# Kernel tuning notes

Hardware: AMD Instinct MI355X
Metric: run time of the kernel (lower is better)

The kernel has to match this reference:

```python
import jax, jax.numpy as jnp
import numpy as np

N = 10000          # nodes
E = 320000         # edges
C = 128            # num_features (channels per irrep)
RB = 8             # radial basis size
NS = 10            # num_species
HID = 64           # radial MLP hidden
NPATH = 5          # TP paths: 0x0->0, 0x1->1, 1x0->1, 1x1->0(dot), 1x1->1(cross)
EPS = 0.17677669529663687  # 1/sqrt(avg_degree=32)


def setup_inputs() -> dict:
    key = jax.random.key(0)
    ks = jax.random.split(key, 20)
    inp = {
        "vectors": jax.random.normal(ks[0], (E, 3), jnp.float32),
        "node_feats": jax.random.normal(ks[1], (N, C * 4), jnp.float32),
        "node_specie": jax.random.randint(ks[2], (N,), 0, NS),
        "radial_embedding": jax.random.normal(ks[3], (E, RB), jnp.float32),
        "senders": jax.random.randint(ks[4], (E,), 0, N),
        "receivers": jax.random.randint(ks[5], (E,), 0, N),
    }
    s = 1.0 / np.sqrt(C)
    inp["W_up_s"] = jax.random.normal(ks[6], (C, C), jnp.float32) * s
    inp["W_up_v"] = jax.random.normal(ks[7], (C, C), jnp.float32) * s
    inp["W_rad1"] = jax.random.normal(ks[8], (RB, HID), jnp.float32) / np.sqrt(RB)
    inp["W_rad2"] = jax.random.normal(ks[9], (HID, NPATH * C), jnp.float32) / np.sqrt(HID)
    inp["W_down_s"] = jax.random.normal(ks[10], (C, C), jnp.float32) * s
    inp["W_down_v"] = jax.random.normal(ks[11], (C, C), jnp.float32) * s
    inp["W_skip_s"] = jax.random.normal(ks[12], (NS, C, C), jnp.float32) * s
    inp["W_skip_v"] = jax.random.normal(ks[13], (NS, C, C), jnp.float32) * s
    inp["W_prod_s"] = jax.random.normal(ks[14], (NS, 3, C), jnp.float32)
    inp["W_prod_v"] = jax.random.normal(ks[15], (NS, 2, C), jnp.float32)
    inp["W_lin_s"] = jax.random.normal(ks[16], (C, C), jnp.float32) * s
    inp["W_lin_v"] = jax.random.normal(ks[17], (C, C), jnp.float32) * s
    inp["W_ro"] = jax.random.normal(ks[18], (C, 1), jnp.float32) * s
    return inp


def _mace_forward(vectors, node_feats, node_specie, radial_embedding, senders,
                  receivers, W_up_s, W_up_v, W_rad1, W_rad2, W_down_s, W_down_v,
                  W_skip_s, W_skip_v, W_prod_s, W_prod_v, W_lin_s, W_lin_v, W_ro):
    n = node_feats.shape[0]
    # split flat mul_ir layout: [C x 0e | C x 1o]
    s = node_feats[:, :C]                      # [N, C]
    v = node_feats[:, C:].reshape(n, C, 3)     # [N, C, 3]

    # --- skip connection (species-indexed linear, first=False) ---
    Ws = W_skip_s[node_specie]                 # [N, C, C]
    Wv = W_skip_v[node_specie]
    sc_s = jnp.einsum('nc,ncd->nd', s, Ws)
    sc_v = jnp.einsum('nci,ncd->ndi', v, Wv)

    # --- interaction: linear_up ---
    h_s = s @ W_up_s
    h_v = jnp.einsum('nci,cd->ndi', v, W_up_v)

    # spherical harmonics (component normalization): Y1 = sqrt(3)*r_hat
    norm = jnp.linalg.norm(vectors, axis=-1, keepdims=True)
    Y1 = jnp.sqrt(3.0) * vectors / (norm + 1e-9)           # [E, 3]

    # radial MLP -> per-edge, per-path, per-channel TP weights
    w = jax.nn.silu(radial_embedding @ W_rad1) @ W_rad2
    w = w.reshape(-1, NPATH, C)                            # [E, 5, C]

    # gather sender features, depthwise ('uvu') CG tensor product with Y
    s_j = h_s[senders]                                     # [E, C]
    v_j = h_v[senders]                                     # [E, C, 3]
    dot = jnp.einsum('eci,ei->ec', v_j, Y1)                # 1o x 1o -> 0e
    crs = jnp.cross(v_j, Y1[:, None, :])                   # 1o x 1o -> 1o
    m_s = w[:, 0] * s_j + w[:, 3] * dot                    # [E, C]
    m_v = (w[:, 1][:, :, None] * s_j[:, :, None] * Y1[:, None, :]
           + w[:, 2][:, :, None] * v_j
           + w[:, 4][:, :, None] * crs)                    # [E, C, 3]

    # scatter to receivers
    agg_s = jax.ops.segment_sum(m_s, receivers, num_segments=n)
    agg_v = jax.ops.segment_sum(m_v, receivers, num_segments=n)

    # linear_down + epsilon scaling
    f_s = (agg_s @ W_down_s) * EPS
    f_v = jnp.einsum('nci,cd->ndi', agg_v, W_down_v) * EPS

    # --- equivariant product basis (correlation=2, symmetric) ---
    # order-1 and order-2 symmetric contractions for (0e, 1o) inputs:
    # scalars: A_s, A_s^2, |A_v|^2 ; vectors: A_v, A_s * A_v
    B_s = jnp.stack([f_s, f_s * f_s, jnp.sum(f_v * f_v, axis=-1)], axis=1)  # [N,3,C]
    B_v = jnp.stack([f_v, f_s[:, :, None] * f_v], axis=1)                    # [N,2,C,3]
    p_s = jnp.einsum('nkc,nkc->nc', B_s, W_prod_s[node_specie])
    p_v = jnp.einsum('nkci,nkc->nci', B_v, W_prod_v[node_specie])
    out_s = p_s @ W_lin_s + sc_s
    out_v = jnp.einsum('nci,cd->ndi', p_v, W_lin_v) + sc_v

    # --- linear readout (not last layer): invariant 0e output ---
    node_outputs = out_s @ W_ro                            # [N, 1]
    new_feats = jnp.concatenate([out_s, out_v.reshape(n, C * 3)], axis=-1)
    return node_outputs, new_feats


def reference(vectors, node_feats, node_specie, radial_embedding, senders,
              receivers, W_up_s, W_up_v, W_rad1, W_rad2, W_down_s, W_down_v,
              W_skip_s, W_skip_v, W_prod_s, W_prod_v, W_lin_s, W_lin_v, W_ro):
    return _mace_forward(vectors, node_feats, node_specie, radial_embedding,
                         senders, receivers, W_up_s, W_up_v, W_rad1, W_rad2,
                         W_down_s, W_down_v, W_skip_s, W_skip_v, W_prod_s,
                         W_prod_v, W_lin_s, W_lin_v, W_ro)
```

## Files before the change

kernel.cpp:

```cpp
#include <hip/hip_runtime.h>
#include <hip/hip_bf16.h>


#define NN 10000
#define EE 320000
#define FEPS 0.17677669529663687f

typedef __attribute__((ext_vector_type(4))) float f32x4;
typedef __attribute__((ext_vector_type(8))) short s16x8;

__device__ __forceinline__ float bflo(unsigned u) { return __uint_as_float(u << 16); }
__device__ __forceinline__ float bfhi(unsigned u) { return __uint_as_float(u & 0xffff0000u); }
__device__ __forceinline__ unsigned short f2bu(float f) {
    unsigned u = __float_as_uint(f);
    return (unsigned short)((u + 0x7FFFu + ((u >> 16) & 1u)) >> 16);
}
__device__ __forceinline__ unsigned pack2(float a, float b) {
    return (unsigned)f2bu(a) | ((unsigned)f2bu(b) << 16);
}
__device__ __forceinline__ s16x8 pack8(float4 a, float4 b) {
    union { s16x8 v; unsigned short u[8]; } r;
    r.u[0] = f2bu(a.x); r.u[1] = f2bu(a.y); r.u[2] = f2bu(a.z); r.u[3] = f2bu(a.w);
    r.u[4] = f2bu(b.x); r.u[5] = f2bu(b.y); r.u[6] = f2bu(b.z); r.u[7] = f2bu(b.w);
    return r.v;
}

#define TWN (26 * 16384)
#define W2N (640 * 64)
#define PREPX 20
#define HISTB 1250
__global__ __launch_bounds__(256) void k_prep_hist(
    const float* __restrict__ Wus, const float* __restrict__ Wuv,
    const float* __restrict__ Wds, const float* __restrict__ Wdv,
    const float* __restrict__ Wls, const float* __restrict__ Wlv,
    const float* __restrict__ Wss, const float* __restrict__ Wsv,
    const float* __restrict__ W_rad2,
    unsigned short* __restrict__ T,
    unsigned short* __restrict__ w2t,
    const int* __restrict__ recv, int* __restrict__ cnt) {
    const int b = blockIdx.x, tid = threadIdx.x;
    if (b < 26) {
        __shared__ unsigned short tr[128][130];
        const int m = b;
        const float* src;
        if (m == 0) src = Wus; else if (m == 1) src = Wuv;
        else if (m == 2) src = Wds; else if (m == 3) src = Wdv;
        else if (m == 4) src = Wls; else if (m == 5) src = Wlv;
        else if (m < 16) src = Wss + (size_t)(m - 6) * 16384;
        else src = Wsv + (size_t)(m - 16) * 16384;
        for (int i = tid; i < 16384; i += 256) {
            const int c = i >> 7, d = i & 127;
            tr[d][c] = f2bu(src[i]);
        }
        __syncthreads();
        unsigned* o32 = (unsigned*)(T + (size_t)m * 16384);
        for (int i = tid; i < 8192; i += 256) {
            const int d = i >> 6, c2 = (i & 63) * 2;
            o32[i] = (unsigned)tr[d][c2] | ((unsigned)tr[d][c2 + 1] << 16);
        }
    } else if (b < 26 + PREPX) {
        for (int i = (b - 26) * 256 + tid; i < W2N; i += PREPX * 256) {
            const int n = i >> 6, k = i & 63;
            w2t[i] = f2bu(W_rad2[k * 640 + n]);
        }
    } else {
        const int e = (b - (26 + PREPX)) * 256 + tid;
        if (e < EE) {
            int r = recv[e];
            r = ((unsigned)r < NN) ? r : 0;
            atomicAdd(&cnt[r], 1);
        }
    }
}

__global__ __launch_bounds__(1024) void k_scan_spec(
    const int* __restrict__ cnt, int* __restrict__ offs, int* __restrict__ cur,
    const int* __restrict__ specie, int* __restrict__ perm,
    int2* __restrict__ tiles, int* __restrict__ ntiles) {
    __shared__ int sums[1024];
    __shared__ int hcnt[10], hbase[10], hcur[10], tbase[11];
    const int t = threadIdx.x;
    const int chunk = (NN + 1023) / 1024;
    const int start = t * chunk;
    int local = 0;
    for (int i = 0; i < chunk; i++) {
        int idx = start + i;
        if (idx < NN) local += cnt[idx];
    }
    sums[t] = local;
    __syncthreads();
    for (int ofs = 1; ofs < 1024; ofs <<= 1) {
        int u = (t >= ofs) ? sums[t - ofs] : 0;
        __syncthreads();
        sums[t] += u;
        __syncthreads();
    }
    int base = (t == 0) ? 0 : sums[t - 1];
    for (int i = 0; i < chunk; i++) {
        int idx = start + i;
        if (idx < NN) {
            offs[idx] = base;
            cur[idx] = base;
            base += cnt[idx];
        }
    }
    if (t == 0) offs[NN] = sums[1023];
    if (t < 10) hcnt[t] = 0;
    __syncthreads();
    for (int n = t; n < NN; n += 1024) {
        int s = specie[n];
        s = ((unsigned)s < 10) ? s : 0;
        atomicAdd(&hcnt[s], 1);
    }
    __syncthreads();
    if (t == 0) {
        int run = 0, tc = 0;
        for (int sp = 0; sp < 10; sp++) {
            hbase[sp] = run; hcur[sp] = run; run += hcnt[sp];
            tbase[sp] = tc;  tc += (hcnt[sp] + 15) >> 4;
        }
        tbase[10] = tc;
        *ntiles = tc;
    }
    __syncthreads();
    const int tc = tbase[10];
    for (int ti = t; ti < tc; ti += 1024) {
        int sp = 0;
        while (sp < 9 && ti >= tbase[sp + 1]) sp++;
        const int b = (ti - tbase[sp]) * 16;
        tiles[ti] = make_int2(hbase[sp] + b, (sp << 8) | min(16, hcnt[sp] - b));
    }
    for (int n = t; n < NN; n += 1024) {
        int s = specie[n];
        s = ((unsigned)s < 10) ? s : 0;
        int slot = atomicAdd(&hcur[s], 1);
        if ((unsigned)slot < NN) perm[slot] = n;
    }
}

__global__ __launch_bounds__(256) void k_fill_pre(
    const int* __restrict__ recv, int* __restrict__ cur, int* __restrict__ csr,
    const float* __restrict__ nf,
    const unsigned short* __restrict__ Tw,
    uint2* __restrict__ h4o) {
    if (blockIdx.x >= 625) {
        const int e = (blockIdx.x - 625) * 256 + threadIdx.x;
        if (e < EE) {
            int r = recv[e];
            r = ((unsigned)r < NN) ? r : 0;
            int slot = atomicAdd(&cur[r], 1);
            if ((unsigned)slot < EE) csr[slot] = e;
        }
        return;
    }
    const int tile = blockIdx.x;
    const int tid = threadIdx.x;
    const int lane = tid & 63, wv = tid >> 6;
    const int col = lane & 15, quad = lane >> 4;
    __shared__ float nfl[16][512];
    {
        const float4* src = (const float4*)(nf + (size_t)tile * 16 * 512);
        float4* dst = (float4*)nfl;
        for (int i = tid; i < 2048; i += 256) dst[i] = src[i];
    }
    __syncthreads();
    const float* rp = nfl[col];
    s16x8 Af[4][4];
#pragma unroll
    for (int kt = 0; kt < 4; kt++) {
        const int ko = kt * 32 + quad * 8;
        const float4 fa = *(const float4*)(rp + ko);
        const float4 fb = *(const float4*)(rp + ko + 4);
        Af[0][kt] = pack8(fa, fb);
#pragma unroll
        for (int i = 0; i < 3; i++) {
            union { s16x8 v; unsigned short u[8]; } A;
#pragma unroll
            for (int j = 0; j < 8; j++) A.u[j] = f2bu(rp[128 + 3 * (ko + j) + i]);
            Af[1 + i][kt] = A.v;
        }
    }
    const unsigned short* Ts = Tw;
    const unsigned short* Tv = Tw + 16384;
#pragma unroll
    for (int nt = 0; nt < 2; nt++) {
        const int d = 32 * wv + 16 * nt + col;
        f32x4 C[4];
#pragma unroll
        for (int m = 0; m < 4; m++) C[m] = (f32x4){0.f, 0.f, 0.f, 0.f};
#pragma unroll
        for (int kt = 0; kt < 4; kt++) {
            const int ko = kt * 32 + quad * 8;
            const s16x8 Bs = *(const s16x8*)&Ts[(size_t)d * 128 + ko];
            const s16x8 Bv = *(const s16x8*)&Tv[(size_t)d * 128 + ko];
            C[0] = __builtin_amdgcn_mfma_f32_16x16x32_bf16(Af[0][kt], Bs, C[0], 0, 0, 0);
#pragma unroll
            for (int i = 0; i < 3; i++)
                C[1 + i] = __builtin_amdgcn_mfma_f32_16x16x32_bf16(Af[1 + i][kt], Bv, C[1 + i], 0, 0, 0);
        }
        const int P = ((d >> 5) << 4) + (d & 15);
        const int half = (d >> 4) & 1;
#pragma unroll
        for (int reg = 0; reg < 4; reg++) {
            const int node = tile * 16 + quad * 4 + reg;
            h4o[((size_t)node * 64 + P) * 2 + half] =
                make_uint2(pack2(C[0][reg], C[1][reg]), pack2(C[2][reg], C[3][reg]));
        }
    }
}

#define EGRID 2560
__global__ __launch_bounds__(256, 2) void k_edge_mfma(
    const float* __restrict__ vectors,
    const float* __restrict__ radial,
    const int* __restrict__ senders,
    const float* __restrict__ W_rad1,
    const unsigned short* __restrict__ w2t,
    const uint4* __restrict__ h4q,
    const int* __restrict__ offs, const int* __restrict__ csr,
    unsigned short* __restrict__ aggb) {
    __shared__ unsigned short w1s[512];
    __shared__ float4 em[3][64];
    __shared__ float radl[3][64][8];
    __shared__ unsigned short hidb[2 * 64 * 72];
    const int tid = threadIdx.x;
    const int lane = tid & 63, wv = tid >> 6;
    const int row = lane & 15, quad = lane >> 4;
    const int sE = tid >> 2, st = tid & 3;
    for (int i = tid; i < 512; i += 256) w1s[i] = f2bu(W_rad1[i]);

    s16x8 Bf[2][5][2];
#pragma unroll
    for (int ti = 0; ti < 2; ti++) {
        const int t = 2 * wv + ti;
#pragma unroll
        for (int p = 0; p < 5; p++) {
            const unsigned short* bp =
                w2t + (size_t)(128 * p + 16 * t + row) * 64 + quad * 8;
            Bf[ti][p][0] = *(const s16x8*)(bp);
            Bf[ti][p][1] = *(const s16x8*)(bp + 32);
        }
    }

    int curN = blockIdx.x, curS = offs[curN], curD = offs[curN + 1] - curS, curC0 = 0;
    int nxtN = curN, nxtS = curS, nxtD = curD, nxtC0 = 0;
    {
        nxtC0 += 64;
        if (nxtC0 >= nxtD) {
            nxtN += EGRID;
            if (nxtN < NN) { nxtS = offs[nxtN]; nxtD = offs[nxtN + 1] - nxtS; }
            nxtC0 = 0;
        }
    }
    int nx2N = nxtN, nx2S = nxtS, nx2D = nxtD, nx2C0 = nxtC0;
    if (nx2N < NN) {
        nx2C0 += 64;
        if (nx2C0 >= nx2D) {
            nx2N += EGRID;
            if (nx2N < NN) { nx2S = offs[nx2N]; nx2D = offs[nx2N + 1] - nx2S; }
            nx2C0 = 0;
        }
    }

    if (st < 2) {
        const int gi = curC0 + sE;
        if (gi < curD) {
            int e = csr[curS + gi];
            e = ((unsigned)e < EE) ? e : 0;
            if (st == 0) {
                int j = senders[e];
                j = ((unsigned)j < NN) ? j : 0;
                const float vx = vectors[e * 3 + 0];
                const float vy = vectors[e * 3 + 1];
                const float vz = vectors[e * 3 + 2];
                const float inr = 1.7320508075688772f /
                    (sqrtf(vx * vx + vy * vy + vz * vz) + 1e-9f);
                em[0][sE] = make_float4(__int_as_float(j), vx * inr, vy * inr, vz * inr);
            } else {
                *(float4*)&radl[0][sE][0] = *(const float4*)(radial + (size_t)e * 8);
                *(float4*)&radl[0][sE][4] = *(const float4*)(radial + (size_t)e * 8 + 4);
            }
        } else {
            if (st == 0) em[0][sE] = make_float4(0.f, 0.f, 0.f, 0.f);
            else {
                *(float4*)&radl[0][sE][0] = make_float4(0.f, 0.f, 0.f, 0.f);
                *(float4*)&radl[0][sE][4] = make_float4(0.f, 0.f, 0.f, 0.f);
            }
        }
    }
    int eReg = -1;
    if (nxtN < NN && st < 2) {
        const int gi = nxtC0 + sE;
        if (gi < nxtD) {
            int e = csr[nxtS + gi];
            eReg = ((unsigned)e < EE) ? e : 0;
        }
    }
    __syncthreads();

    float acc_s[2] = {0.f, 0.f}, av0[2] = {0.f, 0.f},
          av1[2] = {0.f, 0.f}, av2[2] = {0.f, 0.f};
    int cs = 0, hbI = 0;
    while (true) {
        const int ws = (cs == 2) ? 0 : cs + 1;
        const bool hasNxt = (nxtN < NN);
        const float4* emc = em[cs];
        const float* emf = (const float*)emc;
        uint4 hqA[4];
#pragma unroll
        for (int rg = 0; rg < 4; rg++) {
            const int j = __float_as_int(emf[(quad * 4 + rg) * 4]);
            hqA[rg] = h4q[(size_t)j * 64 + (wv << 4) + row];
        }
        bool sv = false;
        float4 ra0 = make_float4(0.f, 0.f, 0.f, 0.f);
        float4 ra1 = make_float4(0.f, 0.f, 0.f, 0.f);
        if (hasNxt && st < 2 && eReg >= 0) {
            sv = true;
            const int e = eReg;
            if (st == 0) {
                int j = senders[e];
                j = ((unsigned)j < NN) ? j : 0;
                ra0 = make_float4(vectors[e * 3 + 0], vectors[e * 3 + 1],
                                  vectors[e * 3 + 2], __int_as_float(j));
            } else {
                ra0 = *(const float4*)(radial + (size_t)e * 8);
                ra1 = *(const float4*)(radial + (size_t)e * 8 + 4);
            }
        }
        int eRegN = -1;
        if (nx2N < NN && st < 2) {
            const int gi = nx2C0 + sE;
            if (gi < nx2D) {
                int e = csr[nx2S + gi];
                eRegN = ((unsigned)e < EE) ? e : 0;
            }
        }
        const int glimC = min(64, curD - curC0);
        {
            const int g16C = (glimC + 15) & ~15;
            unsigned short* hb = hidb + hbI * 4608;
            const int u0 = st * 16;
            if (sE < glimC) {
                float rr[8];
                *(float4*)&rr[0] = *(const float4*)&radl[cs][sE][0];
                *(float4*)&rr[4] = *(const float4*)&radl[cs][sE][4];
#pragma unroll
                for (int h = 0; h < 2; h++) {
                    float a[8];
#pragma unroll
                    for (int u = 0; u < 8; u++) a[u] = 0.f;
#pragma unroll
                    for (int r = 0; r < 8; r++) {
                        const uint4 wa = *(const uint4*)&w1s[r * 64 + u0 + h * 8];
                        const float f = rr[r];
                        a[0] += f * bflo(wa.x); a[1] += f * bfhi(wa.x);
                        a[2] += f * bflo(wa.y); a[3] += f * bfhi(wa.y);
                        a[4] += f * bflo(wa.z); a[5] += f * bfhi(wa.z);
                        a[6] += f * bflo(wa.w); a[7] += f * bfhi(wa.w);
                    }
                    unsigned o[4];
#pragma unroll
                    for (int k = 0; k < 4; k++) {
                        const float s0 = a[2 * k] / (1.f + __expf(-a[2 * k]));
                        const float s1 = a[2 * k + 1] / (1.f + __expf(-a[2 * k + 1]));
                        o[k] = pack2(s0, s1);
                    }
                    *(uint4*)&hb[sE * 72 + u0 + h * 8] = make_uint4(o[0], o[1], o[2], o[3]);
                }
            } else if (sE < g16C) {
                *(uint4*)&hb[sE * 72 + u0] = make_uint4(0, 0, 0, 0);
                *(uint4*)&hb[sE * 72 + u0 + 8] = make_uint4(0, 0, 0, 0);
            }
        }
        if (hasNxt && st < 2) {
            if (st == 0) {
                if (sv) {
                    const float vx = ra0.x, vy = ra0.y, vz = ra0.z;
                    const float inr = 1.7320508075688772f /
                        (sqrtf(vx * vx + vy * vy + vz * vz) + 1e-9f);
                    em[ws][sE] = make_float4(ra0.w, vx * inr, vy * inr, vz * inr);
                } else {
                    em[ws][sE] = make_float4(0.f, 0.f, 0.f, 0.f);
                }
            } else {
                *(float4*)&radl[ws][sE][0] = ra0;
                *(float4*)&radl[ws][sE][4] = ra1;
            }
        }
        __syncthreads();
        {
            __builtin_amdgcn_s_setprio(1);
            const unsigned short* hb = hidb + hbI * 4608;
            for (int g0 = 0; g0 < glimC; g0 += 16) {
                const s16x8 A0 = *(const s16x8*)&hb[(g0 + row) * 72 + quad * 8];
                const s16x8 A1 = *(const s16x8*)&hb[(g0 + row) * 72 + 32 + quad * 8];
                float4 mm[4];
#pragma unroll
                for (int rg = 0; rg < 4; rg++) mm[rg] = emc[g0 + quad * 4 + rg];
                const bool more = (g0 + 16) < glimC;
                uint4 hqB[4];
                if (more) {
#pragma unroll
                    for (int rg = 0; rg < 4; rg++) {
                        const int j = __float_as_int(emf[(g0 + 16 + quad * 4 + rg) * 4]);
                        hqB[rg] = h4q[(size_t)j * 64 + (wv << 4) + row];
                    }
                }
#pragma unroll
                for (int ti = 0; ti < 2; ti++) {
                    float sj[4], a0r[4], a1r[4], a2r[4];
#pragma unroll
                    for (int rg = 0; rg < 4; rg++) {
                        const unsigned wx = ti ? hqA[rg].z : hqA[rg].x;
                        const unsigned wy = ti ? hqA[rg].w : hqA[rg].y;
                        sj[rg] = bflo(wx); a0r[rg] = bfhi(wx);
                        a1r[rg] = bflo(wy); a2r[rg] = bfhi(wy);
                    }
#pragma unroll
                    for (int p = 0; p < 5; p++) {
                        f32x4 z = {0.f, 0.f, 0.f, 0.f};
                        z = __builtin_amdgcn_mfma_f32_16x16x32_bf16(A0, Bf[ti][p][0], z, 0, 0, 0);
                        z = __builtin_amdgcn_mfma_f32_16x16x32_bf16(A1, Bf[ti][p][1], z, 0, 0, 0);
#pragma unroll
                        for (int rg = 0; rg < 4; rg++) {
                            const float w = z[rg];
                            const float y0 = mm[rg].y, y1 = mm[rg].z, y2 = mm[rg].w;
                            if (p == 0) {
                                acc_s[ti] += w * sj[rg];
                            } else if (p == 1) {
                                const float wsj = w * sj[rg];
                                av0[ti] += wsj * y0;
                                av1[ti] += wsj * y1;
                                av2[ti] += wsj * y2;
                            } else if (p == 2) {
                                av0[ti] += w * a0r[rg];
                                av1[ti] += w * a1r[rg];
                                av2[ti] += w * a2r[rg];
                            } else if (p == 3) {
                                acc_s[ti] += w * (a0r[rg] * y0 + a1r[rg] * y1 +
                                                  a2r[rg] * y2);
                            } else {
                                av0[ti] += w * (a1r[rg] * y2 - a2r[rg] * y1);
                                av1[ti] += w * (a2r[rg] * y0 - a0r[rg] * y2);
                                av2[ti] += w * (a0r[rg] * y1 - a1r[rg] * y0);
                            }
                        }
                    }
                }
                if (more) {
#pragma unroll
                    for (int rg = 0; rg < 4; rg++) hqA[rg] = hqB[rg];
                }
            }
            __builtin_amdgcn_s_setprio(0);
            if (curC0 + 64 >= curD) {
#pragma unroll
                for (int ti = 0; ti < 2; ti++) {
                    acc_s[ti] += __shfl_xor(acc_s[ti], 16); acc_s[ti] += __shfl_xor(acc_s[ti], 32);
                    av0[ti] += __shfl_xor(av0[ti], 16);     av0[ti] += __shfl_xor(av0[ti], 32);
                    av1[ti] += __shfl_xor(av1[ti], 16);     av1[ti] += __shfl_xor(av1[ti], 32);
                    av2[ti] += __shfl_xor(av2[ti], 16);     av2[ti] += __shfl_xor(av2[ti], 32);
                }
                if (lane < 16) {
                    unsigned short* og = aggb + (size_t)curN * 512;
#pragma unroll
                    for (int ti = 0; ti < 2; ti++) {
                        const int cc = 16 * (2 * wv + ti) + lane;
                        og[cc] = f2bu(acc_s[ti]);
                        og[128 + cc] = f2bu(av0[ti]);
                        og[256 + cc] = f2bu(av1[ti]);
                        og[384 + cc] = f2bu(av2[ti]);
                    }
                }
                acc_s[0] = acc_s[1] = 0.f; av0[0] = av0[1] = 0.f;
                av1[0] = av1[1] = 0.f;     av2[0] = av2[1] = 0.f;
            }
        }
        if (!hasNxt) break;
        curN = nxtN; curS = nxtS; curD = nxtD; curC0 = nxtC0;
        nxtN = nx2N; nxtS = nx2S; nxtD = nx2D; nxtC0 = nx2C0;
        if (nx2N < NN) {
            nx2C0 += 64;
            if (nx2C0 >= nx2D) {
                nx2N += EGRID;
                if (nx2N < NN) { nx2S = offs[nx2N]; nx2D = offs[nx2N + 1] - nx2S; }
                nx2C0 = 0;
            }
        }
        eReg = eRegN;
        cs = ws; hbI ^= 1;
    }
}

__global__ __launch_bounds__(256) void k_post_mfma(
    const float* __restrict__ nf,
    const unsigned short* __restrict__ aggb,
    const int* __restrict__ perm,
    const int2* __restrict__ tiles,
    const int* __restrict__ ntiles,
    const unsigned short* __restrict__ Tw,
    const float* __restrict__ Wps,
    const float* __restrict__ Wpv,
    const float* __restrict__ Wro,
    float* __restrict__ dout) {
    const int tile = blockIdx.x;
    if (tile >= *ntiles) return;
    const int2 td = tiles[tile];
    const int base = td.x, sp = td.y >> 8, cnt = td.y & 255;
    __shared__ int nodesl[16];
    __shared__ float rol[16];
    __shared__ unsigned short Pl[4][16][128];
    __shared__ float nfl[16][512];
    const int tid = threadIdx.x;
    if (tid < 16) {
        nodesl[tid] = perm[base + ((tid < cnt) ? tid : 0)];
        rol[tid] = 0.f;
    }
    __syncthreads();
    {
        float4* dst = (float4*)nfl;
        for (int i = tid; i < 2048; i += 256) {
            const int r = i >> 7, off = i & 127;
            dst[i] = ((const float4*)(nf + (size_t)nodesl[r] * 512))[off];
        }
    }
    __syncthreads();
    const int lane = tid & 63, wv = tid >> 6;
    const int col = lane & 15, quad = lane >> 4;
    const int aN = nodesl[col];
    const unsigned short* Tds = Tw + (size_t)2 * 16384;
    const unsigned short* Tdv = Tw + (size_t)3 * 16384;
    const unsigned short* Tls = Tw + (size_t)4 * 16384;
    const unsigned short* Tlv = Tw + (size_t)5 * 16384;
    const unsigned short* Tss = Tw + (size_t)(6 + sp) * 16384;
    const unsigned short* Tsv = Tw + (size_t)(16 + sp) * 16384;
    const float* rp = nfl[col];
    f32x4 SC[2][4];
#pragma unroll
    for (int nt = 0; nt < 2; nt++) {
        const int d = 32 * wv + 16 * nt + col;
        f32x4 CF[4];
#pragma unroll
        for (int m = 0; m < 4; m++) CF[m] = (f32x4){0.f, 0.f, 0.f, 0.f};
#pragma unroll
        for (int kt = 0; kt < 4; kt++) {
            const int ko = kt * 32 + quad * 8;
            const s16x8 Bs = *(const s16x8*)&Tds[(size_t)d * 128 + ko];
            const s16x8 Bv = *(const s16x8*)&Tdv[(size_t)d * 128 + ko];
#pragma unroll
            for (int m = 0; m < 4; m++) {
                const s16x8 A = *(const s16x8*)&aggb[(size_t)aN * 512 + m * 128 + ko];
                CF[m] = __builtin_amdgcn_mfma_f32_16x16x32_bf16(A, m ? Bv : Bs, CF[m], 0, 0, 0);
            }
        }
        const float wps0 = Wps[sp * 384 + d];
        const float wps1 = Wps[sp * 384 + 128 + d];
        const float wps2 = Wps[sp * 384 + 256 + d];
        const float wpv0 = Wpv[sp * 256 + d];
        const float wpv1 = Wpv[sp * 256 + 128 + d];
#pragma unroll
        for (int reg = 0; reg < 4; reg++) {
            const float fs = CF[0][reg] * FEPS;
            const float f0 = CF[1][reg] * FEPS;
            const float f1 = CF[2][reg] * FEPS;
            const float f2 = CF[3][reg] * FEPS;
            const float ps = fs * wps0 + fs * fs * wps1 + (f0 * f0 + f1 * f1 + f2 * f2) * wps2;
            const float pb = wpv0 + fs * wpv1;
            const int r = quad * 4 + reg;
            Pl[0][r][d] = f2bu(ps);
            Pl[1][r][d] = f2bu(f0 * pb);
            Pl[2][r][d] = f2bu(f1 * pb);
            Pl[3][r][d] = f2bu(f2 * pb);
        }
        f32x4 CS[4];
#pragma unroll
        for (int m = 0; m < 4; m++) CS[m] = (f32x4){0.f, 0.f, 0.f, 0.f};
#pragma unroll
        for (int kt = 0; kt < 4; kt++) {
            const int ko = kt * 32 + quad * 8;
            const s16x8 Bss = *(const s16x8*)&Tss[(size_t)d * 128 + ko];
            const s16x8 Bsv = *(const s16x8*)&Tsv[(size_t)d * 128 + ko];
            const float4 fa = *(const float4*)(rp + ko);
            const float4 fb = *(const float4*)(rp + ko + 4);
            CS[0] = __builtin_amdgcn_mfma_f32_16x16x32_bf16(pack8(fa, fb), Bss, CS[0], 0, 0, 0);
#pragma unroll
            for (int i = 0; i < 3; i++) {
                union { s16x8 v; unsigned short u[8]; } A;
#pragma unroll
                for (int j = 0; j < 8; j++) A.u[j] = f2bu(rp[128 + 3 * (ko + j) + i]);
                CS[1 + i] = __builtin_amdgcn_mfma_f32_16x16x32_bf16(A.v, Bsv, CS[1 + i], 0, 0, 0);
            }
        }
#pragma unroll
        for (int m = 0; m < 4; m++) SC[nt][m] = CS[m];
    }
    __syncthreads();
#pragma unroll
    for (int nt = 0; nt < 2; nt++) {
        const int d = 32 * wv + 16 * nt + col;
        f32x4 CL[4];
#pragma unroll
        for (int m = 0; m < 4; m++) CL[m] = (f32x4){0.f, 0.f, 0.f, 0.f};
#pragma unroll
        for (int kt = 0; kt < 4; kt++) {
            const int ko = kt * 32 + quad * 8;
            const s16x8 Bls = *(const s16x8*)&Tls[(size_t)d * 128 + ko];
            const s16x8 Blv = *(const s16x8*)&Tlv[(size_t)d * 128 + ko];
#pragma unroll
            for (int m = 0; m < 4; m++) {
                const s16x8 A = *(const s16x8*)&Pl[m][col][ko];
                CL[m] = __builtin_amdgcn_mfma_f32_16x16x32_bf16(A, m ? Blv : Bls, CL[m], 0, 0, 0);
            }
        }
        const float wro = Wro[d];
#pragma unroll
        for (int reg = 0; reg < 4; reg++) {
            const int r = quad * 4 + reg;
            if (r < cnt) {
                const int node = nodesl[r];
                const float outs = CL[0][reg] + SC[nt][0][reg];
                const float o0 = CL[1][reg] + SC[nt][1][reg];
                const float o1 = CL[2][reg] + SC[nt][2][reg];
                const float o2 = CL[3][reg] + SC[nt][3][reg];
                float* o = dout + NN + (size_t)node * 512;
                o[d] = outs;
                o[128 + 3 * d + 0] = o0;
                o[128 + 3 * d + 1] = o1;
                o[128 + 3 * d + 2] = o2;
                atomicAdd(&rol[r], outs * wro);
            }
        }
    }
    __syncthreads();
    if (tid < 16 && tid < cnt) dout[nodesl[tid]] = rol[tid];
}

extern "C" void kernel_launch(void* const* d_in, const int* in_sizes, int n_in,
                              void* d_out, int out_size, void* d_ws, size_t ws_size,
                              hipStream_t stream) {
    const float* vectors    = (const float*)d_in[0];
    const float* node_feats = (const float*)d_in[1];
    const int*   specie     = (const int*)d_in[2];
    const float* radial     = (const float*)d_in[3];
    const int*   senders    = (const int*)d_in[4];
    const int*   receivers  = (const int*)d_in[5];
    const float* W_up_s     = (const float*)d_in[6];
    const float* W_up_v     = (const float*)d_in[7];
    const float* W_rad1     = (const float*)d_in[8];
    const float* W_rad2     = (const float*)d_in[9];
    const float* W_down_s   = (const float*)d_in[10];
    const float* W_down_v   = (const float*)d_in[11];
    const float* W_skip_s   = (const float*)d_in[12];
    const float* W_skip_v   = (const float*)d_in[13];
    const float* W_prod_s   = (const float*)d_in[14];
    const float* W_prod_v   = (const float*)d_in[15];
    const float* W_lin_s    = (const float*)d_in[16];
    const float* W_lin_v    = (const float*)d_in[17];
    const float* W_ro       = (const float*)d_in[18];
    float* out = (float*)d_out;

    char* w = (char*)d_ws;
    auto align256 = [](size_t x) { return (x + 255) & ~(size_t)255; };
    int* cnt  = (int*)w;              w += align256((size_t)NN * 4);
    int* offs = (int*)w;              w += align256((size_t)(NN + 1) * 4);
    int* cur  = (int*)w;              w += align256((size_t)NN * 4);
    int* csr  = (int*)w;              w += align256((size_t)EE * 4);
    uint4* h4q = (uint4*)w;           w += align256((size_t)NN * 64 * 16);
    unsigned short* aggb = (unsigned short*)w;  w += align256((size_t)NN * 512 * 2);
    unsigned short* w2t  = (unsigned short*)w;  w += align256((size_t)W2N * 2);
    unsigned short* Tw   = (unsigned short*)w;  w += align256((size_t)TWN * 2);
    int* perm   = (int*)w;            w += align256((size_t)NN * 4);
    int2* tiles = (int2*)w;           w += align256((size_t)640 * 8);
    int* ntiles = (int*)w;            w += align256(4);

    hipMemsetAsync(cnt, 0, (size_t)NN * 4, stream);
    k_prep_hist<<<26 + PREPX + HISTB, 256, 0, stream>>>(
        W_up_s, W_up_v, W_down_s, W_down_v, W_lin_s, W_lin_v,
        W_skip_s, W_skip_v, W_rad2, Tw, w2t, receivers, cnt);
    k_scan_spec<<<1, 1024, 0, stream>>>(cnt, offs, cur, specie, perm, tiles, ntiles);
    k_fill_pre<<<625 + HISTB, 256, 0, stream>>>(receivers, cur, csr,
                                                node_feats, Tw, (uint2*)h4q);
    k_edge_mfma<<<EGRID, 256, 0, stream>>>(vectors, radial, senders, W_rad1,
                                           w2t, h4q, offs, csr, aggb);
    k_post_mfma<<<640, 256, 0, stream>>>(node_feats, aggb, perm, tiles, ntiles,
                                         Tw, W_prod_s, W_prod_v, W_ro, out);
}
```

Baseline: 393.2 us.

## Deepen edge-kernel software pipeline and move species bucketing out of single-block scan

The per-species histogram and permutation fill move out of the single-block scan kernel into extra blocks of the histogram and CSR-fill kernels, which shortens that serial one-block kernel. The edge kernel gains one more stage of lookahead. The radial-MLP hidden layer for the next chunk is computed before the MFMA work on the current chunk, and the first sender-row gather for the next chunk is prefetched inside the current chunk's loop. This is meant to hide global-load latency and LDS work behind the MFMA phase, at the cost of more registers and more complex indexing and synchronisation.

```diff
diff --git a/kernel.cpp b/kernel.cpp
--- a/kernel.cpp
+++ b/kernel.cpp
@@ -29,6 +29,7 @@
 #define W2N (640 * 64)
 #define PREPX 20
 #define HISTB 1250
+#define SPECB 40
 __global__ __launch_bounds__(256) void k_prep_hist(
     const float* __restrict__ Wus, const float* __restrict__ Wuv,
     const float* __restrict__ Wds, const float* __restrict__ Wdv,
@@ -37,7 +38,8 @@
     const float* __restrict__ W_rad2,
     unsigned short* __restrict__ T,
     unsigned short* __restrict__ w2t,
-    const int* __restrict__ recv, int* __restrict__ cnt) {
+    const int* __restrict__ recv, int* __restrict__ cnt,
+    const int* __restrict__ specie, int* __restrict__ hcnt10) {
     const int b = blockIdx.x, tid = threadIdx.x;
     if (b < 26) {
         __shared__ unsigned short tr[128][130];
@@ -63,22 +65,29 @@
             const int n = i >> 6, k = i & 63;
             w2t[i] = f2bu(W_rad2[k * 640 + n]);
         }
-    } else {
+    } else if (b < 26 + PREPX + HISTB) {
         const int e = (b - (26 + PREPX)) * 256 + tid;
         if (e < EE) {
             int r = recv[e];
             r = ((unsigned)r < NN) ? r : 0;
             atomicAdd(&cnt[r], 1);
         }
+    } else {
+        const int n = (b - (26 + PREPX + HISTB)) * 256 + tid;
+        if (n < NN) {
+            int s = specie[n];
+            s = ((unsigned)s < 10) ? s : 0;
+            atomicAdd(&hcnt10[s], 1);
+        }
     }
 }
 
 __global__ __launch_bounds__(1024) void k_scan_spec(
     const int* __restrict__ cnt, int* __restrict__ offs, int* __restrict__ cur,
-    const int* __restrict__ specie, int* __restrict__ perm,
+    const int* __restrict__ hcnt10, int* __restrict__ gcur,
     int2* __restrict__ tiles, int* __restrict__ ntiles) {
     __shared__ int sums[1024];
-    __shared__ int hcnt[10], hbase[10], hcur[10], tbase[11];
+    __shared__ int hcnt[10], hbase[10], tbase[11];
     const int t = threadIdx.x;
     const int chunk = (NN + 1023) / 1024;
     const int start = t * chunk;
@@ -88,6 +97,7 @@
         if (idx < NN) local += cnt[idx];
     }
     sums[t] = local;
+    if (t < 10) hcnt[t] = hcnt10[t];
     __syncthreads();
     for (int ofs = 1; ofs < 1024; ofs <<= 1) {
         int u = (t >= ofs) ? sums[t - ofs] : 0;
@@ -104,25 +114,18 @@
             base += cnt[idx];
         }
     }
-    if (t == 0) offs[NN] = sums[1023];
-    if (t < 10) hcnt[t] = 0;
-    __syncthreads();
-    for (int n = t; n < NN; n += 1024) {
-        int s = specie[n];
-        s = ((unsigned)s < 10) ? s : 0;
-        atomicAdd(&hcnt[s], 1);
-    }
-    __syncthreads();
     if (t == 0) {
+        offs[NN] = sums[1023];
         int run = 0, tc = 0;
         for (int sp = 0; sp < 10; sp++) {
-            hbase[sp] = run; hcur[sp] = run; run += hcnt[sp];
+            hbase[sp] = run; run += hcnt[sp];
             tbase[sp] = tc;  tc += (hcnt[sp] + 15) >> 4;
         }
         tbase[10] = tc;
         *ntiles = tc;
     }
     __syncthreads();
+    if (t < 10) gcur[t] = hbase[t];
     const int tc = tbase[10];
     for (int ti = t; ti < tc; ti += 1024) {
         int sp = 0;
@@ -130,19 +133,25 @@
         const int b = (ti - tbase[sp]) * 16;
         tiles[ti] = make_int2(hbase[sp] + b, (sp << 8) | min(16, hcnt[sp] - b));
     }
-    for (int n = t; n < NN; n += 1024) {
-        int s = specie[n];
-        s = ((unsigned)s < 10) ? s : 0;
-        int slot = atomicAdd(&hcur[s], 1);
-        if ((unsigned)slot < NN) perm[slot] = n;
-    }
 }
 
 __global__ __launch_bounds__(256) void k_fill_pre(
     const int* __restrict__ recv, int* __restrict__ cur, int* __restrict__ csr,
     const float* __restrict__ nf,
     const unsigned short* __restrict__ Tw,
-    uint2* __restrict__ h4o) {
+    uint2* __restrict__ h4o,
+    const int* __restrict__ specie, int* __restrict__ gcur,
+    int* __restrict__ perm) {
+    if (blockIdx.x >= 625 + HISTB) {
+        const int n = (blockIdx.x - (625 + HISTB)) * 256 + threadIdx.x;
+        if (n < NN) {
+            int s = specie[n];
+            s = ((unsigned)s < 10) ? s : 0;
+            int slot = atomicAdd(&gcur[s], 1);
+            if ((unsigned)slot < NN) perm[slot] = n;
+        }
+        return;
+    }
     if (blockIdx.x >= 625) {
         const int e = (blockIdx.x - 625) * 256 + threadIdx.x;
         if (e < EE) {
@@ -244,83 +253,115 @@
 
     int curN = blockIdx.x, curS = offs[curN], curD = offs[curN + 1] - curS, curC0 = 0;
     int nxtN = curN, nxtS = curS, nxtD = curD, nxtC0 = 0;
-    {
-        nxtC0 += 64;
-        if (nxtC0 >= nxtD) {
-            nxtN += EGRID;
-            if (nxtN < NN) { nxtS = offs[nxtN]; nxtD = offs[nxtN + 1] - nxtS; }
-            nxtC0 = 0;
-        }
-    }
+    { nxtC0 += 64; if (nxtC0 >= nxtD) { nxtN += EGRID;
+        if (nxtN < NN) { nxtS = offs[nxtN]; nxtD = offs[nxtN + 1] - nxtS; } nxtC0 = 0; } }
     int nx2N = nxtN, nx2S = nxtS, nx2D = nxtD, nx2C0 = nxtC0;
-    if (nx2N < NN) {
-        nx2C0 += 64;
-        if (nx2C0 >= nx2D) {
-            nx2N += EGRID;
-            if (nx2N < NN) { nx2S = offs[nx2N]; nx2D = offs[nx2N + 1] - nx2S; }
-            nx2C0 = 0;
-        }
-    }
-
-    if (st < 2) {
-        const int gi = curC0 + sE;
-        if (gi < curD) {
-            int e = csr[curS + gi];
-            e = ((unsigned)e < EE) ? e : 0;
-            if (st == 0) {
-                int j = senders[e];
-                j = ((unsigned)j < NN) ? j : 0;
-                const float vx = vectors[e * 3 + 0];
-                const float vy = vectors[e * 3 + 1];
-                const float vz = vectors[e * 3 + 2];
+    if (nx2N < NN) { nx2C0 += 64; if (nx2C0 >= nx2D) { nx2N += EGRID;
+        if (nx2N < NN) { nx2S = offs[nx2N]; nx2D = offs[nx2N + 1] - nx2S; } nx2C0 = 0; } }
+    int nx3N = nx2N, nx3S = nx2S, nx3D = nx2D, nx3C0 = nx2C0;
+    if (nx3N < NN) { nx3C0 += 64; if (nx3C0 >= nx3D) { nx3N += EGRID;
+        if (nx3N < NN) { nx3S = offs[nx3N]; nx3D = offs[nx3N + 1] - nx3S; } nx3C0 = 0; } }
+
+    auto stage_direct = [&](int N, int S, int D, int C0, int slot) {
+        if (st >= 2) return;
+        const int gi = C0 + sE;
+        const bool v = (N < NN) && (gi < D);
+        int e = 0;
+        if (v) { int ee = csr[S + gi]; e = ((unsigned)ee < EE) ? ee : 0; }
+        if (st == 0) {
+            if (v) {
+                int j = senders[e]; j = ((unsigned)j < NN) ? j : 0;
+                const float vx = vectors[e * 3 + 0], vy = vectors[e * 3 + 1],
+                            vz = vectors[e * 3 + 2];
                 const float inr = 1.7320508075688772f /
                     (sqrtf(vx * vx + vy * vy + vz * vz) + 1e-9f);
-                em[0][sE] = make_float4(__int_as_float(j), vx * inr, vy * inr, vz * inr);
+                em[slot][sE] = make_float4(__int_as_float(j), vx * inr, vy * inr, vz * inr);
             } else {
-                *(float4*)&radl[0][sE][0] = *(const float4*)(radial + (size_t)e * 8);
-                *(float4*)&radl[0][sE][4] = *(const float4*)(radial + (size_t)e * 8 + 4);
+                em[slot][sE] = make_float4(0.f, 0.f, 0.f, 0.f);
             }
         } else {
-            if (st == 0) em[0][sE] = make_float4(0.f, 0.f, 0.f, 0.f);
-            else {
-                *(float4*)&radl[0][sE][0] = make_float4(0.f, 0.f, 0.f, 0.f);
-                *(float4*)&radl[0][sE][4] = make_float4(0.f, 0.f, 0.f, 0.f);
-            }
-        }
-    }
+            if (v) {
+                *(float4*)&radl[slot][sE][0] = *(const float4*)(radial + (size_t)e * 8);
+                *(float4*)&radl[slot][sE][4] = *(const float4*)(radial + (size_t)e * 8 + 4);
+            } else {
+                *(float4*)&radl[slot][sE][0] = make_float4(0.f, 0.f, 0.f, 0.f);
+                *(float4*)&radl[slot][sE][4] = make_float4(0.f, 0.f, 0.f, 0.f);
+            }
+        }
+    };
+
+    auto hid_compute = [&](int slot, int half, int glim) {
+        const int g16 = (glim + 15) & ~15;
+        unsigned short* hb = hidb + half * 4608;
+        const int u0 = st * 16;
+        if (sE < glim) {
+            float rr[8];
+            *(float4*)&rr[0] = *(const float4*)&radl[slot][sE][0];
+            *(float4*)&rr[4] = *(const float4*)&radl[slot][sE][4];
+#pragma unroll
+            for (int h = 0; h < 2; h++) {
+                float a[8];
+#pragma unroll
+                for (int u = 0; u < 8; u++) a[u] = 0.f;
+#pragma unroll
+                for (int r = 0; r < 8; r++) {
+                    const uint4 wa = *(const uint4*)&w1s[r * 64 + u0 + h * 8];
+                    const float f = rr[r];
+                    a[0] += f * bflo(wa.x); a[1] += f * bfhi(wa.x);
+                    a[2] += f * bflo(wa.y); a[3] += f * bfhi(wa.y);
+                    a[4] += f * bflo(wa.z); a[5] += f * bfhi(wa.z);
+                    a[6] += f * bflo(wa.w); a[7] += f * bfhi(wa.w);
+                }
+                unsigned o[4];
+#pragma unroll
+                for (int k = 0; k < 4; k++) {
+                    const float s0 = a[2 * k] / (1.f + __expf(-a[2 * k]));
+                    const float s1 = a[2 * k + 1] / (1.f + __expf(-a[2 * k + 1]));
+                    o[k] = pack2(s0, s1);
+                }
+                *(uint4*)&hb[sE * 72 + u0 + h * 8] = make_uint4(o[0], o[1], o[2], o[3]);
+            }
+        } else if (sE < g16) {
+            *(uint4*)&hb[sE * 72 + u0] = make_uint4(0, 0, 0, 0);
+            *(uint4*)&hb[sE * 72 + u0 + 8] = make_uint4(0, 0, 0, 0);
+        }
+    };
+
+    stage_direct(curN, curS, curD, curC0, 0);
+    stage_direct(nxtN, nxtS, nxtD, nxtC0, 1);
     int eReg = -1;
-    if (nxtN < NN && st < 2) {
-        const int gi = nxtC0 + sE;
-        if (gi < nxtD) {
-            int e = csr[nxtS + gi];
-            eReg = ((unsigned)e < EE) ? e : 0;
+    if (nx2N < NN && st < 2) {
+        const int gi = nx2C0 + sE;
+        if (gi < nx2D) { int e = csr[nx2S + gi]; eReg = ((unsigned)e < EE) ? e : 0; }
+    }
+    __syncthreads();
+    hid_compute(0, 0, min(64, curD - curC0));
+    uint4 hqA[4];
+    {
+        const float* emf0 = (const float*)em[0];
+#pragma unroll
+        for (int rg = 0; rg < 4; rg++) {
+            const int j = __float_as_int(emf0[(quad * 4 + rg) * 4]);
+            hqA[rg] = h4q[(size_t)j * 64 + (wv << 4) + row];
         }
     }
     __syncthreads();
 
     float acc_s[2] = {0.f, 0.f}, av0[2] = {0.f, 0.f},
           av1[2] = {0.f, 0.f}, av2[2] = {0.f, 0.f};
-    int cs = 0, hbI = 0;
+    int cs = 0, hb = 0;
     while (true) {
-        const int ws = (cs == 2) ? 0 : cs + 1;
-        const bool hasNxt = (nxtN < NN);
-        const float4* emc = em[cs];
-        const float* emf = (const float*)emc;
-        uint4 hqA[4];
-#pragma unroll
-        for (int rg = 0; rg < 4; rg++) {
-            const int j = __float_as_int(emf[(quad * 4 + rg) * 4]);
-            hqA[rg] = h4q[(size_t)j * 64 + (wv << 4) + row];
-        }
+        const int ns = (cs == 2) ? 0 : cs + 1;
+        const int ws2 = (ns == 2) ? 0 : ns + 1;
+        const bool hasNxt = nxtN < NN, has2 = nx2N < NN, has3 = nx3N < NN;
         bool sv = false;
         float4 ra0 = make_float4(0.f, 0.f, 0.f, 0.f);
         float4 ra1 = make_float4(0.f, 0.f, 0.f, 0.f);
-        if (hasNxt && st < 2 && eReg >= 0) {
+        if (has2 && st < 2 && eReg >= 0) {
             sv = true;
             const int e = eReg;
             if (st == 0) {
-                int j = senders[e];
-                j = ((unsigned)j < NN) ? j : 0;
+                int j = senders[e]; j = ((unsigned)j < NN) ? j : 0;
                 ra0 = make_float4(vectors[e * 3 + 0], vectors[e * 3 + 1],
                                   vectors[e * 3 + 2], __int_as_float(j));
             } else {
@@ -329,72 +370,45 @@
             }
         }
         int eRegN = -1;
-        if (nx2N < NN && st < 2) {
-            const int gi = nx2C0 + sE;
-            if (gi < nx2D) {
-                int e = csr[nx2S + gi];
-                eRegN = ((unsigned)e < EE) ? e : 0;
-            }
-        }
-        const int glimC = min(64, curD - curC0);
-        {
-            const int g16C = (glimC + 15) & ~15;
-            unsigned short* hb = hidb + hbI * 4608;
-            const int u0 = st * 16;
-            if (sE < glimC) {
-                float rr[8];
-                *(float4*)&rr[0] = *(const float4*)&radl[cs][sE][0];
-                *(float4*)&rr[4] = *(const float4*)&radl[cs][sE][4];
-#pragma unroll
-                for (int h = 0; h < 2; h++) {
-                    float a[8];
-#pragma unroll
-                    for (int u = 0; u < 8; u++) a[u] = 0.f;
-#pragma unroll
-                    for (int r = 0; r < 8; r++) {
-                        const uint4 wa = *(const uint4*)&w1s[r * 64 + u0 + h * 8];
-                        const float f = rr[r];
-                        a[0] += f * bflo(wa.x); a[1] += f * bfhi(wa.x);
-                        a[2] += f * bflo(wa.y); a[3] += f * bfhi(wa.y);
-                        a[4] += f * bflo(wa.z); a[5] += f * bfhi(wa.z);
-                        a[6] += f * bflo(wa.w); a[7] += f * bfhi(wa.w);
-                    }
-                    unsigned o[4];
-#pragma unroll
-                    for (int k = 0; k < 4; k++) {
-                        const float s0 = a[2 * k] / (1.f + __expf(-a[2 * k]));
-                        const float s1 = a[2 * k + 1] / (1.f + __expf(-a[2 * k + 1]));
-                        o[k] = pack2(s0, s1);
-                    }
-                    *(uint4*)&hb[sE * 72 + u0 + h * 8] = make_uint4(o[0], o[1], o[2], o[3]);
-                }
-            } else if (sE < g16C) {
-                *(uint4*)&hb[sE * 72 + u0] = make_uint4(0, 0, 0, 0);
-                *(uint4*)&hb[sE * 72 + u0 + 8] = make_uint4(0, 0, 0, 0);
-            }
-        }
-        if (hasNxt && st < 2) {
+        if (has3 && st < 2) {
+            const int gi = nx3C0 + sE;
+            if (gi < nx3D) { int e = csr[nx3S + gi]; eRegN = ((unsigned)e < EE) ? e : 0; }
+        }
+        if (hasNxt) hid_compute(ns, hb ^ 1, min(64, nxtD - nxtC0));
+        if (has2 && st < 2) {
             if (st == 0) {
                 if (sv) {
                     const float vx = ra0.x, vy = ra0.y, vz = ra0.z;
                     const float inr = 1.7320508075688772f /
                         (sqrtf(vx * vx + vy * vy + vz * vz) + 1e-9f);
-                    em[ws][sE] = make_float4(ra0.w, vx * inr, vy * inr, vz * inr);
+                    em[ws2][sE] = make_float4(ra0.w, vx * inr, vy * inr, vz * inr);
                 } else {
-                    em[ws][sE] = make_float4(0.f, 0.f, 0.f, 0.f);
+                    em[ws2][sE] = make_float4(0.f, 0.f, 0.f, 0.f);
                 }
             } else {
-                *(float4*)&radl[ws][sE][0] = ra0;
-                *(float4*)&radl[ws][sE][4] = ra1;
-            }
-        }
-        __syncthreads();
+                *(float4*)&radl[ws2][sE][0] = ra0;
+                *(float4*)&radl[ws2][sE][4] = ra1;
+            }
+        }
+        const int glimC = min(64, curD - curC0);
+        __builtin_amdgcn_s_setprio(1);
         {
-            __builtin_amdgcn_s_setprio(1);
-            const unsigned short* hb = hidb + hbI * 4608;
+            const unsigned short* hbp = hidb + hb * 4608;
+            const float4* emc = em[cs];
+            const float* emf = (const float*)emc;
+            const float* emfn = (const float*)em[ns];
+            if (glimC == 0) {
+                if (hasNxt) {
+#pragma unroll
+                    for (int rg = 0; rg < 4; rg++) {
+                        const int j = __float_as_int(emfn[(quad * 4 + rg) * 4]);
+                        hqA[rg] = h4q[(size_t)j * 64 + (wv << 4) + row];
+                    }
+                }
+            } else
             for (int g0 = 0; g0 < glimC; g0 += 16) {
-                const s16x8 A0 = *(const s16x8*)&hb[(g0 + row) * 72 + quad * 8];
-                const s16x8 A1 = *(const s16x8*)&hb[(g0 + row) * 72 + 32 + quad * 8];
+                const s16x8 A0 = *(const s16x8*)&hbp[(g0 + row) * 72 + quad * 8];
+                const s16x8 A1 = *(const s16x8*)&hbp[(g0 + row) * 72 + 32 + quad * 8];
                 float4 mm[4];
 #pragma unroll
                 for (int rg = 0; rg < 4; rg++) mm[rg] = emc[g0 + quad * 4 + rg];
@@ -404,6 +418,12 @@
 #pragma unroll
                     for (int rg = 0; rg < 4; rg++) {
                         const int j = __float_as_int(emf[(g0 + 16 + quad * 4 + rg) * 4]);
+                        hqB[rg] = h4q[(size_t)j * 64 + (wv << 4) + row];
+                    }
+                } else if (hasNxt) {
+#pragma unroll
+                    for (int rg = 0; rg < 4; rg++) {
+                        const int j = __float_as_int(emfn[(quad * 4 + rg) * 4]);
                         hqB[rg] = h4q[(size_t)j * 64 + (wv << 4) + row];
                     }
                 }
@@ -448,48 +468,48 @@
                         }
                     }
                 }
-                if (more) {
-#pragma unroll
-                    for (int rg = 0; rg < 4; rg++) hqA[rg] = hqB[rg];
+#pragma unroll
+                for (int rg = 0; rg < 4; rg++) hqA[rg] = hqB[rg];
+            }
+        }
+        __builtin_amdgcn_s_setprio(0);
+        if (curC0 + 64 >= curD) {
+#pragma unroll
+            for (int ti = 0; ti < 2; ti++) {
+                acc_s[ti] += __shfl_xor(acc_s[ti], 16); acc_s[ti] += __shfl_xor(acc_s[ti], 32);
+                av0[ti] += __shfl_xor(av0[ti], 16);     av0[ti] += __shfl_xor(av0[ti], 32);
+                av1[ti] += __shfl_xor(av1[ti], 16);     av1[ti] += __shfl_xor(av1[ti], 32);
+                av2[ti] += __shfl_xor(av2[ti], 16);     av2[ti] += __shfl_xor(av2[ti], 32);
+            }
+            if (lane < 16) {
+                unsigned short* og = aggb + (size_t)curN * 512;
+#pragma unroll
+                for (int ti = 0; ti < 2; ti++) {
+                    const int cc = 16 * (2 * wv + ti) + lane;
+                    og[cc] = f2bu(acc_s[ti]);
+                    og[128 + cc] = f2bu(av0[ti]);
+                    og[256 + cc] = f2bu(av1[ti]);
+                    og[384 + cc] = f2bu(av2[ti]);
                 }
             }
-            __builtin_amdgcn_s_setprio(0);
-            if (curC0 + 64 >= curD) {
-#pragma unroll
-                for (int ti = 0; ti < 2; ti++) {
-                    acc_s[ti] += __shfl_xor(acc_s[ti], 16); acc_s[ti] += __shfl_xor(acc_s[ti], 32);
-                    av0[ti] += __shfl_xor(av0[ti], 16);     av0[ti] += __shfl_xor(av0[ti], 32);
-                    av1[ti] += __shfl_xor(av1[ti], 16);     av1[ti] += __shfl_xor(av1[ti], 32);
-                    av2[ti] += __shfl_xor(av2[ti], 16);     av2[ti] += __shfl_xor(av2[ti], 32);
-                }
-                if (lane < 16) {
-                    unsigned short* og = aggb + (size_t)curN * 512;
-#pragma unroll
-                    for (int ti = 0; ti < 2; ti++) {
-                        const int cc = 16 * (2 * wv + ti) + lane;
-                        og[cc] = f2bu(acc_s[ti]);
-                        og[128 + cc] = f2bu(av0[ti]);
-                        og[256 + cc] = f2bu(av1[ti]);
-                        og[384 + cc] = f2bu(av2[ti]);
-                    }
-                }
-                acc_s[0] = acc_s[1] = 0.f; av0[0] = av0[1] = 0.f;
-                av1[0] = av1[1] = 0.f;     av2[0] = av2[1] = 0.f;
-            }
+            acc_s[0] = acc_s[1] = 0.f; av0[0] = av0[1] = 0.f;
+            av1[0] = av1[1] = 0.f;     av2[0] = av2[1] = 0.f;
         }
         if (!hasNxt) break;
         curN = nxtN; curS = nxtS; curD = nxtD; curC0 = nxtC0;
         nxtN = nx2N; nxtS = nx2S; nxtD = nx2D; nxtC0 = nx2C0;
-        if (nx2N < NN) {
-            nx2C0 += 64;
-            if (nx2C0 >= nx2D) {
-                nx2N += EGRID;
-                if (nx2N < NN) { nx2S = offs[nx2N]; nx2D = offs[nx2N + 1] - nx2S; }
-                nx2C0 = 0;
+        nx2N = nx3N; nx2S = nx3S; nx2D = nx3D; nx2C0 = nx3C0;
+        if (nx3N < NN) {
+            nx3C0 += 64;
+            if (nx3C0 >= nx3D) {
+                nx3N += EGRID;
+                if (nx3N < NN) { nx3S = offs[nx3N]; nx3D = offs[nx3N + 1] - nx3S; }
+                nx3C0 = 0;
             }
         }
         eReg = eRegN;
-        cs = ws; hbI ^= 1;
+        cs = ns; hb ^= 1;
+        __syncthreads();
     }
 }
 
@@ -663,6 +683,8 @@
     char* w = (char*)d_ws;
     auto align256 = [](size_t x) { return (x + 255) & ~(size_t)255; };
     int* cnt  = (int*)w;              w += align256((size_t)NN * 4);
+    int* hcnt10 = (int*)w;            w += 256;
+    int* gcur   = (int*)w;            w += 256;
     int* offs = (int*)w;              w += align256((size_t)(NN + 1) * 4);
     int* cur  = (int*)w;              w += align256((size_t)NN * 4);
     int* csr  = (int*)w;              w += align256((size_t)EE * 4);
@@ -674,13 +696,13 @@
     int2* tiles = (int2*)w;           w += align256((size_t)640 * 8);
     int* ntiles = (int*)w;            w += align256(4);
 
-    hipMemsetAsync(cnt, 0, (size_t)NN * 4, stream);
-    k_prep_hist<<<26 + PREPX + HISTB, 256, 0, stream>>>(
+    hipMemsetAsync(cnt, 0, align256((size_t)NN * 4) + 256, stream);
+    k_prep_hist<<<26 + PREPX + HISTB + SPECB, 256, 0, stream>>>(
         W_up_s, W_up_v, W_down_s, W_down_v, W_lin_s, W_lin_v,
-        W_skip_s, W_skip_v, W_rad2, Tw, w2t, receivers, cnt);
-    k_scan_spec<<<1, 1024, 0, stream>>>(cnt, offs, cur, specie, perm, tiles, ntiles);
-    k_fill_pre<<<625 + HISTB, 256, 0, stream>>>(receivers, cur, csr,
-                                                node_feats, Tw, (uint2*)h4q);
+        W_skip_s, W_skip_v, W_rad2, Tw, w2t, receivers, cnt, specie, hcnt10);
+    k_scan_spec<<<1, 1024, 0, stream>>>(cnt, offs, cur, hcnt10, gcur, tiles, ntiles);
+    k_fill_pre<<<625 + HISTB + SPECB, 256, 0, stream>>>(
+        receivers, cur, csr, node_feats, Tw, (uint2*)h4q, specie, gcur, perm);
     k_edge_mfma<<<EGRID, 256, 0, stream>>>(vectors, radial, senders, W_rad1,
                                            w2t, h4q, offs, csr, aggb);
     k_post_mfma<<<640, 256, 0, stream>>>(node_feats, aggb, perm, tiles, ntiles,
```

Result: slower. 595.0 us (+51.3%).
